# Kernel optimization log

Measured on AMD Instinct MI355X. Metric: run time of the kernel, lower is better.

Reference implementation:

```python
import jax, jax.numpy as jnp
import numpy as np

N_QUBITS = 22
DIM = 2 ** N_QUBITS


def setup_inputs() -> dict:
    key = jax.random.key(0)
    k1, k2, k3, k4 = jax.random.split(key, 4)
    state = jax.random.normal(k1, (DIM,), dtype=jnp.float32)
    state = state / jnp.linalg.norm(state)
    rabi = jax.random.uniform(k2, (N_QUBITS,), dtype=jnp.float32)
    detune = jax.random.uniform(k3, (N_QUBITS,), dtype=jnp.float32)
    # U = triu(normal^2, k=1) flattened upper triangle -> interaction strengths
    U_params = jax.random.normal(k4, (N_QUBITS * (N_QUBITS - 1) // 2,), dtype=jnp.float32) ** 2
    return {"state": state, "rabi": rabi, "detune": detune, "U_params": U_params}


def reference(state, rabi, detune, U_params):
    # H|psi> = sum_i (rabi_i/2) X_i |psi> + sum_i (-detune_i) N_i |psi>
    #        + sum_{i<j} U_ij N_i N_j |psi>
    n = rabi.shape[0]
    dim = state.shape[0]
    # bit value of qubit i for each basis index k (qubit 0 = most significant,
    # matching state.reshape((2,)*n) axis ordering)
    idx = jnp.arange(dim, dtype=jnp.uint32)
    shifts = jnp.arange(n - 1, -1, -1, dtype=jnp.uint32)
    bits = ((idx[:, None] >> shifts[None, :]) & 1).astype(state.dtype)  # [dim, n]
    iu, ju = np.triu_indices(n, k=1)
    Umat = jnp.zeros((n, n), dtype=state.dtype).at[iu, ju].set(U_params)
    # diagonal part: detuning (Number ops) + pairwise interactions (N_i N_j)
    diag = bits @ (-detune) + jnp.sum((bits @ Umat) * bits, axis=1)  # [dim]
    out = diag * state
    # off-diagonal Rabi part: X_i flips qubit i
    st = state.reshape((2,) * n)
    for i in range(n):
        out = out + (0.5 * rabi[i]) * jnp.flip(st, axis=i).reshape(-1)
    return out
```

## Files before the change

### kernel.cpp

```cpp
#include <hip/hip_runtime.h>


#define THREADS 512
#define NBLK 512

typedef float fvec4 __attribute__((ext_vector_type(4)));

__device__ __forceinline__ int uidx(int i, int j) {
    return i * (43 - i) / 2 + (j - i - 1);
}

__global__ __launch_bounds__(THREADS, 4) void ryd_kernel(
        const float* __restrict__ state, const float* __restrict__ rabi,
        const float* __restrict__ detune, const float* __restrict__ U,
        float* __restrict__ out) {
    __shared__ float4 tileS[2048];
    __shared__ __align__(16) float dloS[2048];
    __shared__ float Us[231];
    __shared__ float dets[22];
    __shared__ float CJ[4][11];
    __shared__ float S4v[4];

    const float4* __restrict__ sF4 = (const float4*)state;
    float4* __restrict__ oF4 = (float4*)out;
    const unsigned t = threadIdx.x;
    const unsigned blk = blockIdx.x;
    const unsigned tile = ((blk & 7u) << 6) | (blk >> 3);
    const unsigned tbase = tile * 2048u;

    if (t < 231u) Us[t] = U[t];
    else if (t < 253u) dets[t - 231u] = detune[t - 231u];

    float4 vreg[4];
#pragma unroll
    for (int c = 0; c < 4; ++c)
        vreg[c] = sF4[tbase + t + 512u * (unsigned)c];
    float4 pgl[2][3];
#pragma unroll
    for (int b = 6; b < 9; ++b)
        pgl[0][b - 6] = sF4[(tbase + t) ^ (2048u << b)];

    __syncthreads();

    {
        float base = 0.f, R9 = 0.f, R10 = 0.f;
#pragma unroll
        for (int j2 = 0; j2 < 9; ++j2) {
            if ((t >> j2) & 1u) {
                base -= dets[21 - j2];
#pragma unroll
                for (int j1 = 0; j1 < j2; ++j1)
                    if ((t >> j1) & 1u) base += Us[uidx(21 - j2, 21 - j1)];
                R9  += Us[uidx(12, 21 - j2)];
                R10 += Us[uidx(11, 21 - j2)];
            }
        }
        const float w9  = -dets[12];
        const float w10 = -dets[11];
        const float u910 = Us[uidx(11, 12)];
        dloS[t]         = base;
        dloS[t + 512u]  = base + w9 + R9;
        dloS[t + 1024u] = base + w10 + R10;
        dloS[t + 1536u] = base + w9 + R9 + w10 + R10 + u910;
    }
    if (t < 44u) {
        const int c = (int)t / 11, j = (int)t % 11;
        const unsigned h = (tile << 2) | (unsigned)c;
        float cc = 0.f;
        for (int jh = 0; jh < 11; ++jh)
            if ((h >> jh) & 1u) cc += Us[uidx(10 - jh, 21 - j)];
        CJ[c][j] = cc;
    } else if (t < 48u) {
        const int c = (int)t - 44;
        const unsigned h = (tile << 2) | (unsigned)c;
        float s = 0.f;
        for (int j2 = 0; j2 < 11; ++j2) {
            if ((h >> j2) & 1u) {
                s -= dets[10 - j2];
                for (int j1 = 0; j1 < j2; ++j1)
                    if ((h >> j1) & 1u) s += Us[uidx(10 - j2, 10 - j1)];
            }
        }
        S4v[c] = s;
    }

#pragma unroll
    for (int c = 0; c < 4; ++c)
        tileS[t + 512u * (unsigned)c] = vreg[c];
    __syncthreads();

    const float r0 = 0.5f * rabi[21];
    const float r1 = 0.5f * rabi[20];
    const float r11 = 0.5f * rabi[10];
    const float r12 = 0.5f * rabi[9];
    float cb[9];
#pragma unroll
    for (int b = 0; b < 9; ++b) cb[b] = 0.5f * rabi[8 - b];

    const float4 dl = ((const float4*)dloS)[t];

#pragma unroll
    for (int c = 0; c < 4; ++c) {
        const unsigned f = t + 512u * (unsigned)c;
        const unsigned F = tbase + f;
        float4 pg[6];
#pragma unroll
        for (int b = 0; b < 6; ++b)
            pg[b] = sF4[F ^ (2048u << b)];
        if (c < 3) {
#pragma unroll
            for (int b = 6; b < 9; ++b)
                pgl[(c + 1) & 1][b - 6] = sF4[(F + 512u) ^ (2048u << b)];
        }

        float cj[11];
#pragma unroll
        for (int j = 0; j < 11; ++j) cj[j] = CJ[c][j];
        float s = S4v[c];
#pragma unroll
        for (int j = 0; j < 9; ++j)
            s += ((t >> j) & 1u) ? cj[j + 2] : 0.f;
        const float4 v = vreg[c];
        const float d0 = s + dl.x;
        const float d1 = s + cj[0] + dl.y;
        const float d2 = s + cj[1] + dl.z;
        const float d3 = s + cj[0] + cj[1] + dl.w;
        float4 acc;
        acc.x = d0 * v.x; acc.y = d1 * v.y; acc.z = d2 * v.z; acc.w = d3 * v.w;
        acc.x += r0 * v.y; acc.y += r0 * v.x; acc.z += r0 * v.w; acc.w += r0 * v.z;
        acc.x += r1 * v.z; acc.y += r1 * v.w; acc.z += r1 * v.x; acc.w += r1 * v.y;
        {
            const float4 pa = vreg[c ^ 1];
            const float4 pb = vreg[c ^ 2];
            acc.x += r11 * pa.x; acc.y += r11 * pa.y;
            acc.z += r11 * pa.z; acc.w += r11 * pa.w;
            acc.x += r12 * pb.x; acc.y += r12 * pb.y;
            acc.z += r12 * pb.z; acc.w += r12 * pb.w;
        }
#pragma unroll
        for (int b = 2; b <= 10; ++b) {
            const float rb = 0.5f * rabi[21 - b];
            const float4 p = tileS[f ^ (1u << (b - 2))];
            acc.x += rb * p.x; acc.y += rb * p.y; acc.z += rb * p.z; acc.w += rb * p.w;
        }
#pragma unroll
        for (int b = 0; b < 6; ++b) {
            acc.x += cb[b] * pg[b].x; acc.y += cb[b] * pg[b].y;
            acc.z += cb[b] * pg[b].z; acc.w += cb[b] * pg[b].w;
        }
#pragma unroll
        for (int q = 0; q < 3; ++q) {
            const float4 p = pgl[c & 1][q];
            acc.x += cb[6 + q] * p.x; acc.y += cb[6 + q] * p.y;
            acc.z += cb[6 + q] * p.z; acc.w += cb[6 + q] * p.w;
        }
        union { float4 s4; fvec4 v4; } u;
        u.s4 = acc;
        __builtin_nontemporal_store(u.v4, reinterpret_cast<fvec4*>(oF4 + F));
    }
}

extern "C" void kernel_launch(void* const* d_in, const int* in_sizes, int n_in,
                              void* d_out, int out_size, void* d_ws, size_t ws_size,
                              hipStream_t stream) {
    const float* state  = (const float*)d_in[0];
    const float* rabi   = (const float*)d_in[1];
    const float* detune = (const float*)d_in[2];
    const float* U      = (const float*)d_in[3];
    float* out = (float*)d_out;
    (void)in_sizes; (void)n_in; (void)out_size; (void)d_ws; (void)ws_size;

    hipLaunchKernelGGL(ryd_kernel, dim3(NBLK), dim3(THREADS), 0, stream,
                       state, rabi, detune, U, out);
}
```

Before: 20.94 us.

## Split Hamiltonian apply into high-bit and low-bit kernels using shared-memory tiles

Replaces the single kernel, which gathered high-qubit flip partners with strided global loads, with two passes. The first loads a strided tile covering the high qubits into shared memory, computes the diagonal term and the high-bit flips, and writes partial output. The second loads contiguous tiles, reads back the partial output, and adds the low-bit flips. This removes redundant global gathers but adds a second launch and an extra read and write of the output buffer.

```diff
diff --git a/kernel.cpp b/kernel.cpp
--- a/kernel.cpp
+++ b/kernel.cpp
@@ -10,153 +10,172 @@
     return i * (43 - i) / 2 + (j - i - 1);
 }
 
-__global__ __launch_bounds__(THREADS, 4) void ryd_kernel(
+__global__ __launch_bounds__(THREADS, 4) void ryd_hi_kernel(
         const float* __restrict__ state, const float* __restrict__ rabi,
         const float* __restrict__ detune, const float* __restrict__ U,
         float* __restrict__ out) {
     __shared__ float4 tileS[2048];
-    __shared__ __align__(16) float dloS[2048];
+    __shared__ float T1s[512];
+    __shared__ __align__(16) float C4s[512][4];
+    __shared__ __align__(16) float T2s[16];
     __shared__ float Us[231];
     __shared__ float dets[22];
-    __shared__ float CJ[4][11];
-    __shared__ float S4v[4];
 
     const float4* __restrict__ sF4 = (const float4*)state;
     float4* __restrict__ oF4 = (float4*)out;
     const unsigned t = threadIdx.x;
-    const unsigned blk = blockIdx.x;
-    const unsigned tile = ((blk & 7u) << 6) | (blk >> 3);
-    const unsigned tbase = tile * 2048u;
+    const unsigned B = blockIdx.x;
+    const unsigned q = t & 3u;
 
     if (t < 231u) Us[t] = U[t];
     else if (t < 253u) dets[t - 231u] = detune[t - 231u];
 
     float4 vreg[4];
+    unsigned Gidx[4];
 #pragma unroll
-    for (int c = 0; c < 4; ++c)
-        vreg[c] = sF4[tbase + t + 512u * (unsigned)c];
-    float4 pgl[2][3];
-#pragma unroll
-    for (int b = 6; b < 9; ++b)
-        pgl[0][b - 6] = sF4[(tbase + t) ^ (2048u << b)];
-
+    for (int c = 0; c < 4; ++c) {
+        const unsigned lf = t + 512u * (unsigned)c;
+        const unsigned hi = lf >> 2;
+        const unsigned G = (hi << 11) | (B << 2) | q;
+        Gidx[c] = G;
+        vreg[c] = sF4[G];
+    }
     __syncthreads();
 
     {
-        float base = 0.f, R9 = 0.f, R10 = 0.f;
+        const unsigned h = t;
+        float d = 0.f;
 #pragma unroll
-        for (int j2 = 0; j2 < 9; ++j2) {
-            if ((t >> j2) & 1u) {
-                base -= dets[21 - j2];
+        for (int j = 0; j < 9; ++j) {
+            if ((h >> j) & 1u) {
+                d -= dets[8 - j];
 #pragma unroll
-                for (int j1 = 0; j1 < j2; ++j1)
-                    if ((t >> j1) & 1u) base += Us[uidx(21 - j2, 21 - j1)];
-                R9  += Us[uidx(12, 21 - j2)];
-                R10 += Us[uidx(11, 21 - j2)];
+                for (int j1 = 0; j1 < j; ++j1)
+                    if ((h >> j1) & 1u) d += Us[uidx(8 - j, 8 - j1)];
+#pragma unroll
+                for (int i = 0; i < 9; ++i)
+                    if ((B >> i) & 1u) d += Us[uidx(8 - j, 17 - i)];
             }
         }
-        const float w9  = -dets[12];
-        const float w10 = -dets[11];
-        const float u910 = Us[uidx(11, 12)];
-        dloS[t]         = base;
-        dloS[t + 512u]  = base + w9 + R9;
-        dloS[t + 1024u] = base + w10 + R10;
-        dloS[t + 1536u] = base + w9 + R9 + w10 + R10 + u910;
+        T1s[t] = d;
+#pragma unroll
+        for (int j = 0; j < 4; ++j) {
+            float cc = 0.f;
+#pragma unroll
+            for (int jh = 0; jh < 9; ++jh)
+                if ((h >> jh) & 1u) cc += Us[uidx(8 - jh, 21 - j)];
+            C4s[t][j] = cc;
+        }
     }
-    if (t < 44u) {
-        const int c = (int)t / 11, j = (int)t % 11;
-        const unsigned h = (tile << 2) | (unsigned)c;
-        float cc = 0.f;
-        for (int jh = 0; jh < 11; ++jh)
-            if ((h >> jh) & 1u) cc += Us[uidx(10 - jh, 21 - j)];
-        CJ[c][j] = cc;
-    } else if (t < 48u) {
-        const int c = (int)t - 44;
-        const unsigned h = (tile << 2) | (unsigned)c;
+    if (t < 16u) {
+        const unsigned m4 = t;
         float s = 0.f;
-        for (int j2 = 0; j2 < 11; ++j2) {
-            if ((h >> j2) & 1u) {
-                s -= dets[10 - j2];
-                for (int j1 = 0; j1 < j2; ++j1)
-                    if ((h >> j1) & 1u) s += Us[uidx(10 - j2, 10 - j1)];
+        for (int j = 0; j < 4; ++j) {
+            if ((m4 >> j) & 1u) {
+                s -= dets[21 - j];
+                for (int j1 = 0; j1 < j; ++j1)
+                    if ((m4 >> j1) & 1u) s += Us[uidx(21 - j, 21 - j1)];
+                for (int i = 0; i < 9; ++i)
+                    if ((B >> i) & 1u) s += Us[uidx(17 - i, 21 - j)];
             }
         }
-        S4v[c] = s;
+        T2s[t] = s;
     }
-
+    float Smid = 0.f;
+#pragma unroll
+    for (int i2 = 0; i2 < 9; ++i2) {
+        if ((B >> i2) & 1u) {
+            Smid -= dets[17 - i2];
+#pragma unroll
+            for (int i1 = 0; i1 < i2; ++i1)
+                if ((B >> i1) & 1u) Smid += Us[uidx(17 - i2, 17 - i1)];
+        }
+    }
 #pragma unroll
     for (int c = 0; c < 4; ++c)
         tileS[t + 512u * (unsigned)c] = vreg[c];
     __syncthreads();
 
-    const float r0 = 0.5f * rabi[21];
-    const float r1 = 0.5f * rabi[20];
+    float cb[9];
+#pragma unroll
+    for (int j = 0; j < 9; ++j) cb[j] = 0.5f * rabi[8 - j];
+    const float4 t2 = ((const float4*)T2s)[q];
+
+#pragma unroll
+    for (int c = 0; c < 4; ++c) {
+        const unsigned lf = t + 512u * (unsigned)c;
+        const unsigned hi = lf >> 2;
+        const float4 v = vreg[c];
+        const float T1h = T1s[hi];
+        const float4 c4 = *(const float4*)C4s[hi];
+        const float base = Smid + T1h + ((q & 1u) ? c4.z : 0.f) + ((q & 2u) ? c4.w : 0.f);
+        const float d0 = base + t2.x;
+        const float d1 = base + c4.x + t2.y;
+        const float d2 = base + c4.y + t2.z;
+        const float d3 = base + c4.x + c4.y + t2.w;
+        float4 acc;
+        acc.x = d0 * v.x; acc.y = d1 * v.y; acc.z = d2 * v.z; acc.w = d3 * v.w;
+#pragma unroll
+        for (int j = 0; j < 9; ++j) {
+            const float4 p = tileS[lf ^ (4u << j)];
+            acc.x += cb[j] * p.x; acc.y += cb[j] * p.y;
+            acc.z += cb[j] * p.z; acc.w += cb[j] * p.w;
+        }
+        oF4[Gidx[c]] = acc;
+    }
+}
+
+__global__ __launch_bounds__(THREADS, 4) void ryd_lo_kernel(
+        const float* __restrict__ state, const float* __restrict__ rabi,
+        float* __restrict__ out) {
+    __shared__ float4 tileS[2048];
+    const float4* __restrict__ sF4 = (const float4*)state;
+    float4* __restrict__ oF4 = (float4*)out;
+    const unsigned t = threadIdx.x;
+    const unsigned tbase = blockIdx.x * 2048u;
+
+    float4 vreg[4], prev[4];
+#pragma unroll
+    for (int c = 0; c < 4; ++c) {
+        vreg[c] = sF4[tbase + t + 512u * (unsigned)c];
+        prev[c] = oF4[tbase + t + 512u * (unsigned)c];
+    }
+#pragma unroll
+    for (int c = 0; c < 4; ++c)
+        tileS[t + 512u * (unsigned)c] = vreg[c];
+    __syncthreads();
+
+    const float r0  = 0.5f * rabi[21];
+    const float r1  = 0.5f * rabi[20];
     const float r11 = 0.5f * rabi[10];
     const float r12 = 0.5f * rabi[9];
-    float cb[9];
+    float rb[9];
 #pragma unroll
-    for (int b = 0; b < 9; ++b) cb[b] = 0.5f * rabi[8 - b];
-
-    const float4 dl = ((const float4*)dloS)[t];
+    for (int j = 0; j < 9; ++j) rb[j] = 0.5f * rabi[19 - j];
 
 #pragma unroll
     for (int c = 0; c < 4; ++c) {
         const unsigned f = t + 512u * (unsigned)c;
-        const unsigned F = tbase + f;
-        float4 pg[6];
-#pragma unroll
-        for (int b = 0; b < 6; ++b)
-            pg[b] = sF4[F ^ (2048u << b)];
-        if (c < 3) {
-#pragma unroll
-            for (int b = 6; b < 9; ++b)
-                pgl[(c + 1) & 1][b - 6] = sF4[(F + 512u) ^ (2048u << b)];
-        }
-
-        float cj[11];
-#pragma unroll
-        for (int j = 0; j < 11; ++j) cj[j] = CJ[c][j];
-        float s = S4v[c];
-#pragma unroll
-        for (int j = 0; j < 9; ++j)
-            s += ((t >> j) & 1u) ? cj[j + 2] : 0.f;
         const float4 v = vreg[c];
-        const float d0 = s + dl.x;
-        const float d1 = s + cj[0] + dl.y;
-        const float d2 = s + cj[1] + dl.z;
-        const float d3 = s + cj[0] + cj[1] + dl.w;
-        float4 acc;
-        acc.x = d0 * v.x; acc.y = d1 * v.y; acc.z = d2 * v.z; acc.w = d3 * v.w;
+        float4 acc = prev[c];
         acc.x += r0 * v.y; acc.y += r0 * v.x; acc.z += r0 * v.w; acc.w += r0 * v.z;
         acc.x += r1 * v.z; acc.y += r1 * v.w; acc.z += r1 * v.x; acc.w += r1 * v.y;
         {
             const float4 pa = vreg[c ^ 1];
             const float4 pb = vreg[c ^ 2];
-            acc.x += r11 * pa.x; acc.y += r11 * pa.y;
-            acc.z += r11 * pa.z; acc.w += r11 * pa.w;
-            acc.x += r12 * pb.x; acc.y += r12 * pb.y;
-            acc.z += r12 * pb.z; acc.w += r12 * pb.w;
+            acc.x += r11 * pa.x; acc.y += r11 * pa.y; acc.z += r11 * pa.z; acc.w += r11 * pa.w;
+            acc.x += r12 * pb.x; acc.y += r12 * pb.y; acc.z += r12 * pb.z; acc.w += r12 * pb.w;
         }
 #pragma unroll
-        for (int b = 2; b <= 10; ++b) {
-            const float rb = 0.5f * rabi[21 - b];
-            const float4 p = tileS[f ^ (1u << (b - 2))];
-            acc.x += rb * p.x; acc.y += rb * p.y; acc.z += rb * p.z; acc.w += rb * p.w;
-        }
-#pragma unroll
-        for (int b = 0; b < 6; ++b) {
-            acc.x += cb[b] * pg[b].x; acc.y += cb[b] * pg[b].y;
-            acc.z += cb[b] * pg[b].z; acc.w += cb[b] * pg[b].w;
-        }
-#pragma unroll
-        for (int q = 0; q < 3; ++q) {
-            const float4 p = pgl[c & 1][q];
-            acc.x += cb[6 + q] * p.x; acc.y += cb[6 + q] * p.y;
-            acc.z += cb[6 + q] * p.z; acc.w += cb[6 + q] * p.w;
+        for (int j = 0; j < 9; ++j) {
+            const float4 p = tileS[f ^ (1u << j)];
+            acc.x += rb[j] * p.x; acc.y += rb[j] * p.y;
+            acc.z += rb[j] * p.z; acc.w += rb[j] * p.w;
         }
         union { float4 s4; fvec4 v4; } u;
         u.s4 = acc;
-        __builtin_nontemporal_store(u.v4, reinterpret_cast<fvec4*>(oF4 + F));
+        __builtin_nontemporal_store(
+            u.v4, reinterpret_cast<fvec4*>(oF4 + tbase + f));
     }
 }
 
@@ -170,6 +189,8 @@
     float* out = (float*)d_out;
     (void)in_sizes; (void)n_in; (void)out_size; (void)d_ws; (void)ws_size;
 
-    hipLaunchKernelGGL(ryd_kernel, dim3(NBLK), dim3(THREADS), 0, stream,
+    hipLaunchKernelGGL(ryd_hi_kernel, dim3(NBLK), dim3(THREADS), 0, stream,
                        state, rabi, detune, U, out);
+    hipLaunchKernelGGL(ryd_lo_kernel, dim3(NBLK), dim3(THREADS), 0, stream,
+                       state, rabi, out);
 }
```

Result: slower. 25.31 us (+20.9%).
